# Kernel optimization log

Measured on AMD Instinct MI355X. Metric: run time of the kernel, lower is better.

## Reference

```python
import jax, jax.numpy as jnp
import numpy as np

NUM_PERIODS = 24


def setup_inputs() -> dict:
    key = jax.random.key(0)
    ks = jax.random.split(key, 12)
    B, N, F, H, E = 32, 1024, 128, 64, 16
    scale = 1.0 / np.sqrt(F)
    inp = {
        "input_features": jax.random.normal(ks[0], (B, N, F), jnp.float32),
        "cycle_indices": jax.random.randint(ks[1], (B,), 0, NUM_PERIODS, jnp.int64),
        "weight": jax.random.normal(ks[2], (F, F), jnp.float32) * scale,
        "bias": jnp.zeros((F,), jnp.float32),
        "src_emb": jax.random.normal(ks[3], (NUM_PERIODS, N, H), jnp.float32) * 0.1,
        "tgt_emb": jax.random.normal(ks[4], (NUM_PERIODS, N, H), jnp.float32) * 0.1,
        "env_W": jax.random.normal(ks[5], (E, H), jnp.float32) * (1.0 / np.sqrt(E)),
        "env_b": jnp.zeros((H,), jnp.float32),
        "res_W": jax.random.normal(ks[6], (F, F), jnp.float32) * scale,
        "res_b": jnp.zeros((F,), jnp.float32),
        "static_adj": (jax.random.uniform(ks[7], (N, N)) < 0.05).astype(jnp.float32),
        "env_features": jax.random.normal(ks[8], (N, E), jnp.float32),
    }
    return inp


def reference(input_features, cycle_indices, weight, bias, src_emb, tgt_emb,
              env_W, env_b, res_W, res_b, static_adj, env_features):
    # env encoder: Linear + ReLU (dropout is identity at inference)
    env_emb = jax.nn.relu(env_features @ env_W + env_b)            # [N, H]

    # per-period adaptive adjacency, masked by static sparsity pattern
    src = src_emb + env_emb                                        # [P, N, H]
    tgt = tgt_emb + env_emb                                        # [P, N, H]
    scores = jnp.einsum('pnh,pmh->pnm', src, tgt)                  # [P, N, N]
    adj = jax.nn.relu(scores) * static_adj                         # [P, N, N]

    period = (cycle_indices % NUM_PERIODS).astype(jnp.int32)       # [B]
    adj_b = adj[period]                                            # [B, N, N]

    support = jnp.einsum('bnd,dm->bnm', input_features, weight)    # [B, N, F]
    convolved = jnp.einsum('bnm,bmf->bnf', adj_b, support) + bias  # [B, N, F]

    residual = jax.nn.relu(input_features @ res_W + res_b)         # [B, N, F]
    return jax.nn.relu(convolved + residual)
```

## Files before the change

kernel.cpp:

```cpp
#include <hip/hip_runtime.h>
#include <hip/hip_bf16.h>

#define NPER 24
#define B_ 32
#define N_ 1024
#define F_ 128
#define H_ 64
#define E_ 16

typedef __attribute__((ext_vector_type(8))) short short8;
typedef __attribute__((ext_vector_type(4))) float f32x4;

#define GLD16(g, l) __builtin_amdgcn_global_load_lds( \
    (const __attribute__((address_space(1))) void*)(g), \
    (__attribute__((address_space(3))) void*)(l), 16, 0, 0)

static __device__ __forceinline__ unsigned short f2bf(float x) {
    union { float f; unsigned u; } v; v.f = x;
    unsigned r = v.u + 0x7fffu + ((v.u >> 16) & 1u);
    return (unsigned short)(r >> 16);
}
static __device__ __forceinline__ float bf2f(unsigned short h) {
    union { unsigned u; float f; } v; v.u = ((unsigned)h) << 16; return v.f;
}
static __device__ __forceinline__ unsigned short f2bf_hw(float x) {
    __hip_bfloat16 h = __float2bfloat16(x);
    return *(unsigned short*)&h;
}

__global__ __launch_bounds__(256) void prep_all(
    const float* __restrict__ src_emb, const float* __restrict__ tgt_emb,
    const float* __restrict__ env_features, const float* __restrict__ env_W,
    const float* __restrict__ env_b,
    const float* __restrict__ adj, const float* __restrict__ W,
    const float* __restrict__ rW, const float* __restrict__ x,
    unsigned short* __restrict__ src_bf, unsigned short* __restrict__ tgt_bf,
    unsigned short* __restrict__ adj_bf, unsigned short* __restrict__ Wt,
    unsigned short* __restrict__ rWt, unsigned short* __restrict__ x_bf)
{
    const int bid = blockIdx.x;
    if (bid < 1536) {
        const int g   = bid >> 8;
        const int idx = (bid & 255) * 256 + threadIdx.x;
        const int n = idx >> 6, h = idx & 63;
        float e = env_b[h];
#pragma unroll
        for (int k = 0; k < E_; ++k)
            e = fmaf(env_features[n * E_ + k], env_W[k * H_ + h], e);
        e = fmaxf(e, 0.f);
#pragma unroll
        for (int pp = 0; pp < 4; ++pp) {
            const size_t off = (size_t)(g * 4 + pp) * (N_ * H_) + idx;
            src_bf[off] = f2bf(src_emb[off] + e);
            tgt_bf[off] = f2bf(tgt_emb[off] + e);
        }
    } else if (bid < 2560) {
        const size_t i = ((size_t)(bid - 1536) * 256 + threadIdx.x) * 4;
        float4 v = *(const float4*)(adj + i);
        ushort4 o;
        o.x = f2bf(v.x); o.y = f2bf(v.y); o.z = f2bf(v.z); o.w = f2bf(v.w);
        *(ushort4*)(adj_bf + i) = o;
    } else if (bid < 2688) {
        const int idx = (bid - 2560) * 256 + threadIdx.x;
        const int which = idx >> 14, j = idx & 16383;
        const int f = j >> 7, d = j & 127;
        if (which == 0) Wt[f * 128 + d]  = f2bf(W[d * 128 + f]);
        else            rWt[f * 128 + d] = f2bf(rW[d * 128 + f]);
    } else {
        const size_t i = ((size_t)(bid - 2688) * 256 + threadIdx.x) * 4;
        float4 v = *(const float4*)(x + i);
        ushort4 o;
        o.x = f2bf(v.x); o.y = f2bf(v.y); o.z = f2bf(v.z); o.w = f2bf(v.w);
        *(ushort4*)(x_bf + i) = o;
    }
}

__global__ __launch_bounds__(256, 2) void gemm2_mfma(
    const unsigned short* __restrict__ x_bf,
    const unsigned short* __restrict__ Wt,
    const unsigned short* __restrict__ rWt,
    const float* __restrict__ rb,
    unsigned short* __restrict__ supT,
    unsigned short* __restrict__ resid)
{
    __shared__ unsigned short s_w[128 * 128] __attribute__((aligned(16)));
    __shared__ unsigned short s_r[128 * 128] __attribute__((aligned(16)));
    __shared__ unsigned short s_x[64 * 128]  __attribute__((aligned(16)));

    const int t = threadIdx.x, w = t >> 6, l = t & 63;
    const int ln = l & 15, kb = l >> 4;
    const size_t row0 = (size_t)blockIdx.x * 64;
    const int b   = (int)(row0 >> 10);
    const int mg0 = (int)(row0 & 1023);

#pragma unroll
    for (int j = 0; j < 8; ++j) {
        const int te = j * 256 + t;
        const int r = te >> 4, c = te & 15;
        GLD16(Wt  + (size_t)r * 128 + (c ^ (r & 7)) * 8, &s_w[te * 8]);
        GLD16(rWt + (size_t)r * 128 + (c ^ (r & 7)) * 8, &s_r[te * 8]);
    }
#pragma unroll
    for (int j = 0; j < 4; ++j) {
        const int te = j * 256 + t;
        const int r = te >> 4, c = te & 15;
        GLD16(x_bf + row0 * 128 + (size_t)r * 128 + (c ^ (r & 7)) * 8,
              &s_x[te * 8]);
    }
    asm volatile("s_waitcnt vmcnt(0) lgkmcnt(0)" ::: "memory");
    __builtin_amdgcn_s_barrier();

    f32x4 accS[8], accR[8];
#pragma unroll
    for (int q = 0; q < 8; ++q) { accS[q] = (f32x4){0,0,0,0}; accR[q] = (f32x4){0,0,0,0}; }

    const int xr = w * 16 + ln;
#pragma unroll
    for (int k = 0; k < 4; ++k) {
        short8 xa = *(const short8*)(&s_x[xr * 128 + ((k * 4 + kb) ^ (xr & 7)) * 8]);
#pragma unroll
        for (int ff = 0; ff < 8; ++ff) {
            const int fr = ff * 16 + ln;
            short8 wa = *(const short8*)(&s_w[fr * 128 + ((k * 4 + kb) ^ (fr & 7)) * 8]);
            short8 wb = *(const short8*)(&s_r[fr * 128 + ((k * 4 + kb) ^ (fr & 7)) * 8]);
            accS[ff] = __builtin_amdgcn_mfma_f32_16x16x32_bf16(wa, xa, accS[ff], 0, 0, 0);
            accR[ff] = __builtin_amdgcn_mfma_f32_16x16x32_bf16(xa, wb, accR[ff], 0, 0, 0);
        }
    }

#pragma unroll
    for (int ff = 0; ff < 8; ++ff) {
        const int m = mg0 + w * 16 + ln;
#pragma unroll
        for (int i = 0; i < 4; ++i) {
            const int f = ff * 16 + kb * 4 + i;
            supT[((size_t)b * 128 + f) * 1024 + m] = f2bf(accS[ff][i]);
        }
    }
#pragma unroll
    for (int ff = 0; ff < 8; ++ff) {
        const int f = ff * 16 + ln;
        const float rbf = rb[f];
#pragma unroll
        for (int i = 0; i < 4; ++i) {
            const size_t row = row0 + w * 16 + kb * 4 + i;
            resid[row * 128 + f] = f2bf(fmaxf(accR[ff][i] + rbf, 0.f));
        }
    }
}

__global__ __launch_bounds__(256, 2) void conv_mfma(
    const unsigned short* __restrict__ src_bf,
    const unsigned short* __restrict__ tgt_bf,
    const unsigned short* __restrict__ adj_bf,
    const unsigned short* __restrict__ supT,
    const unsigned short* __restrict__ resid,
    const float* __restrict__ bias,
    const int* __restrict__ cyc,
    float* __restrict__ out)
{
    __shared__ unsigned short s_tgt[2][64 * 64] __attribute__((aligned(16)));
    __shared__ unsigned short s_sup[2][128 * 64] __attribute__((aligned(16)));
    __shared__ unsigned short s_a[64][72] __attribute__((aligned(16)));

    const int i = blockIdx.x;
    const int work = (i & 7) * 64 + (i >> 3);
    const int b  = work >> 4;
    const int n0 = (work & 15) * 64;

    const int t = threadIdx.x, w = t >> 6, l = t & 63;
    const int ln = l & 15, kb = l >> 4;
    const int p = ((cyc[b] % NPER) + NPER) % NPER;

    const int sn = w >> 1, sm = w & 1;
    const int cf = w;

    short8 sfrag[2][2];
#pragma unroll
    for (int nt = 0; nt < 2; ++nt)
#pragma unroll
        for (int k2 = 0; k2 < 2; ++k2)
            sfrag[nt][k2] = *(const short8*)(
                src_bf + ((size_t)p * N_ + n0 + sn * 32 + nt * 16 + ln) * H_ + k2 * 32 + kb * 8);

    const unsigned short* tgtg = tgt_bf + (size_t)p * N_ * H_;
    const unsigned short* supg = supT + (size_t)b * F_ * N_;

    f32x4 acc[4][2];
#pragma unroll
    for (int q = 0; q < 4; ++q)
#pragma unroll
        for (int fb = 0; fb < 2; ++fb) acc[q][fb] = (f32x4){0, 0, 0, 0};

    auto stage = [&](int buf, int m0) {
#pragma unroll
        for (int j = 0; j < 2; ++j) {
            const int te = j * 256 + t;
            const int r = te >> 3, c = te & 7;
            GLD16(tgtg + (size_t)(m0 + r) * H_ + (c ^ (r & 7)) * 8,
                  &s_tgt[buf][te * 8]);
        }
#pragma unroll
        for (int j = 0; j < 4; ++j) {
            const int te = j * 256 + t;
            const int r = te >> 3, c = te & 7;
            GLD16(supg + (size_t)r * N_ + m0 + (c ^ (r & 7)) * 8,
                  &s_sup[buf][te * 8]);
        }
    };

    auto loadAdj = [&](int m0, ushort4 (&av)[2][2]) {
#pragma unroll
        for (int nt = 0; nt < 2; ++nt)
#pragma unroll
            for (int mt = 0; mt < 2; ++mt)
                av[nt][mt] = *(const ushort4*)(
                    adj_bf + (size_t)(n0 + sn * 32 + nt * 16 + ln) * N_
                           + m0 + sm * 32 + mt * 16 + kb * 4);
    };

    auto score = [&](int buf, const ushort4 (&av)[2][2]) {
        short8 tf[2][2];
#pragma unroll
        for (int mt = 0; mt < 2; ++mt)
#pragma unroll
            for (int k2 = 0; k2 < 2; ++k2) {
                const int trow = sm * 32 + mt * 16 + ln;
                tf[mt][k2] = *(const short8*)(
                    &s_tgt[buf][trow * 64 + ((k2 * 4 + kb) ^ (trow & 7)) * 8]);
            }
#pragma unroll
        for (int nt = 0; nt < 2; ++nt)
#pragma unroll
            for (int mt = 0; mt < 2; ++mt) {
                f32x4 c = (f32x4){0, 0, 0, 0};
                c = __builtin_amdgcn_mfma_f32_16x16x32_bf16(tf[mt][0], sfrag[nt][0], c, 0, 0, 0);
                c = __builtin_amdgcn_mfma_f32_16x16x32_bf16(tf[mt][1], sfrag[nt][1], c, 0, 0, 0);
                const int nl = sn * 32 + nt * 16 + ln;
                const int ml = sm * 32 + mt * 16 + kb * 4;
                const ushort4 a = av[nt][mt];
                uint2 q;
                q.x = (unsigned)f2bf_hw(fmaxf(c[0], 0.f) * bf2f(a.x))
                    | ((unsigned)f2bf_hw(fmaxf(c[1], 0.f) * bf2f(a.y)) << 16);
                q.y = (unsigned)f2bf_hw(fmaxf(c[2], 0.f) * bf2f(a.z))
                    | ((unsigned)f2bf_hw(fmaxf(c[3], 0.f) * bf2f(a.w)) << 16);
                *(uint2*)(&s_a[nl][ml]) = q;
            }
    };

    auto conv = [&](int buf) {
#pragma unroll
        for (int ks = 0; ks < 2; ++ks) {
            short8 bfrag[2];
#pragma unroll
            for (int fb = 0; fb < 2; ++fb) {
                const int frow = cf * 32 + fb * 16 + ln;
                bfrag[fb] = *(const short8*)(
                    &s_sup[buf][frow * 64 + ((ks * 4 + kb) ^ (frow & 7)) * 8]);
            }
#pragma unroll
            for (int nt2 = 0; nt2 < 4; ++nt2) {
                short8 af = *(const short8*)(&s_a[nt2 * 16 + ln][ks * 32 + kb * 8]);
#pragma unroll
                for (int fb = 0; fb < 2; ++fb)
                    acc[nt2][fb] = __builtin_amdgcn_mfma_f32_16x16x32_bf16(
                        af, bfrag[fb], acc[nt2][fb], 0, 0, 0);
            }
        }
    };

    auto bar_lgkm = []() {
        asm volatile("s_waitcnt lgkmcnt(0)" ::: "memory");
        __builtin_amdgcn_s_barrier();
    };
    auto bar_vm0 = []() {
        asm volatile("s_waitcnt vmcnt(0) lgkmcnt(0)" ::: "memory");
        __builtin_amdgcn_s_barrier();
    };

    ushort4 avA[2][2], avB[2][2];

    stage(0, 0);
    loadAdj(0, avA);
    bar_vm0();

    for (int tt = 0; tt < 16; tt += 2) {
        stage(1, (tt + 1) * 64);
        loadAdj((tt + 1) * 64, avB);
        score(0, avA);
        bar_lgkm();
        conv(0);
        bar_vm0();

        if (tt + 2 < 16) {
            stage(0, (tt + 2) * 64);
            loadAdj((tt + 2) * 64, avA);
        }
        score(1, avB);
        bar_lgkm();
        conv(1);
        bar_vm0();
    }

#pragma unroll
    for (int nt2 = 0; nt2 < 4; ++nt2)
#pragma unroll
    for (int fb = 0; fb < 2; ++fb) {
        const int f = cf * 32 + fb * 16 + ln;
        const float bi = bias[f];
#pragma unroll
        for (int ii = 0; ii < 4; ++ii) {
            const int n = n0 + nt2 * 16 + kb * 4 + ii;
            const size_t o = ((size_t)b * N_ + n) * F_ + f;
            out[o] = fmaxf(acc[nt2][fb][ii] + bi + bf2f(resid[o]), 0.f);
        }
    }
}

extern "C" void kernel_launch(void* const* d_in, const int* in_sizes, int n_in,
                              void* d_out, int out_size, void* d_ws, size_t ws_size,
                              hipStream_t stream) {
    const float* input_features = (const float*)d_in[0];
    const int*   cycle_indices  = (const int*)  d_in[1];
    const float* weight         = (const float*)d_in[2];
    const float* bias           = (const float*)d_in[3];
    const float* src_emb        = (const float*)d_in[4];
    const float* tgt_emb        = (const float*)d_in[5];
    const float* env_W          = (const float*)d_in[6];
    const float* env_b          = (const float*)d_in[7];
    const float* res_W          = (const float*)d_in[8];
    const float* res_b          = (const float*)d_in[9];
    const float* static_adj     = (const float*)d_in[10];
    const float* env_features   = (const float*)d_in[11];
    float* out = (float*)d_out;

    char* wsb = (char*)d_ws;
    unsigned short* src_bf = (unsigned short*)wsb;
    unsigned short* tgt_bf = src_bf + (size_t)NPER * N_ * H_;
    unsigned short* Wt     = tgt_bf + (size_t)NPER * N_ * H_;
    unsigned short* rWt    = Wt + 16384;
    unsigned short* supT   = rWt + 16384;
    unsigned short* resid  = supT + (size_t)B_ * F_ * N_;
    unsigned short* adj_bf = resid + (size_t)B_ * N_ * F_;
    unsigned short* x_bf   = adj_bf + (size_t)N_ * N_;

    prep_all<<<6784, 256, 0, stream>>>(
        src_emb, tgt_emb, env_features, env_W, env_b,
        static_adj, weight, res_W, input_features,
        src_bf, tgt_bf, adj_bf, Wt, rWt, x_bf);

    gemm2_mfma<<<(B_ * N_) / 64, 256, 0, stream>>>(
        x_bf, Wt, rWt, res_b, supT, resid);

    conv_mfma<<<512, 256, 0, stream>>>(
        src_bf, tgt_bf, adj_bf, supT, resid, bias, cycle_indices, out);
}
```

Measured before the change: 54.58 us.

## Shrink conv K-tile to 32 with 4-stage LDS ring and vmcnt-based prefetch

The fused score+conv kernel now uses 32-wide m tiles instead of 64 and keeps four LDS stages instead of two. Loads for tile c+2 are issued while tile c is computed, and a partial s_waitcnt vmcnt replaces full vmcnt(0) drains. Launch bounds move to 3 blocks per SM so that more waves fit per CU. This aims to hide global-load latency and raise occupancy, at the cost of twice as many barriers per unit of work, smaller MFMA batches per stage, and reliance on exact vmcnt accounting.

```diff
diff --git a/kernel.cpp b/kernel.cpp
--- a/kernel.cpp
+++ b/kernel.cpp
@@ -149,7 +149,7 @@
     }
 }
 
-__global__ __launch_bounds__(256, 2) void conv_mfma(
+__global__ __launch_bounds__(256, 3) void conv_mfma(
     const unsigned short* __restrict__ src_bf,
     const unsigned short* __restrict__ tgt_bf,
     const unsigned short* __restrict__ adj_bf,
@@ -159,9 +159,9 @@
     const int* __restrict__ cyc,
     float* __restrict__ out)
 {
-    __shared__ unsigned short s_tgt[2][64 * 64] __attribute__((aligned(16)));
-    __shared__ unsigned short s_sup[2][128 * 64] __attribute__((aligned(16)));
-    __shared__ unsigned short s_a[64][72] __attribute__((aligned(16)));
+    __shared__ unsigned short s_tgt[4][32 * 64]  __attribute__((aligned(16)));
+    __shared__ unsigned short s_sup[4][128 * 32] __attribute__((aligned(16)));
+    __shared__ unsigned short s_a[64][36]        __attribute__((aligned(16)));
 
     const int i = blockIdx.x;
     const int work = (i & 7) * 64 + (i >> 3);
@@ -193,113 +193,112 @@
         for (int fb = 0; fb < 2; ++fb) acc[q][fb] = (f32x4){0, 0, 0, 0};
 
     auto stage = [&](int buf, int m0) {
+        {
+            const int r = t >> 3, c = t & 7;
+            GLD16(tgtg + (size_t)(m0 + r) * H_ + (c ^ (r & 7)) * 8,
+                  &s_tgt[buf][t * 8]);
+        }
 #pragma unroll
         for (int j = 0; j < 2; ++j) {
             const int te = j * 256 + t;
-            const int r = te >> 3, c = te & 7;
-            GLD16(tgtg + (size_t)(m0 + r) * H_ + (c ^ (r & 7)) * 8,
-                  &s_tgt[buf][te * 8]);
-        }
-#pragma unroll
-        for (int j = 0; j < 4; ++j) {
-            const int te = j * 256 + t;
-            const int r = te >> 3, c = te & 7;
-            GLD16(supg + (size_t)r * N_ + m0 + (c ^ (r & 7)) * 8,
+            const int r = te >> 2, c = te & 3;
+            GLD16(supg + (size_t)r * N_ + m0 + (c ^ ((r >> 1) & 3)) * 8,
                   &s_sup[buf][te * 8]);
         }
     };
 
-    auto loadAdj = [&](int m0, ushort4 (&av)[2][2]) {
+    auto loadAdj = [&](int m0, ushort4 (&av)[2]) {
 #pragma unroll
         for (int nt = 0; nt < 2; ++nt)
-#pragma unroll
-            for (int mt = 0; mt < 2; ++mt)
-                av[nt][mt] = *(const ushort4*)(
-                    adj_bf + (size_t)(n0 + sn * 32 + nt * 16 + ln) * N_
-                           + m0 + sm * 32 + mt * 16 + kb * 4);
-    };
-
-    auto score = [&](int buf, const ushort4 (&av)[2][2]) {
-        short8 tf[2][2];
-#pragma unroll
-        for (int mt = 0; mt < 2; ++mt)
-#pragma unroll
-            for (int k2 = 0; k2 < 2; ++k2) {
-                const int trow = sm * 32 + mt * 16 + ln;
-                tf[mt][k2] = *(const short8*)(
-                    &s_tgt[buf][trow * 64 + ((k2 * 4 + kb) ^ (trow & 7)) * 8]);
-            }
-#pragma unroll
-        for (int nt = 0; nt < 2; ++nt)
-#pragma unroll
-            for (int mt = 0; mt < 2; ++mt) {
-                f32x4 c = (f32x4){0, 0, 0, 0};
-                c = __builtin_amdgcn_mfma_f32_16x16x32_bf16(tf[mt][0], sfrag[nt][0], c, 0, 0, 0);
-                c = __builtin_amdgcn_mfma_f32_16x16x32_bf16(tf[mt][1], sfrag[nt][1], c, 0, 0, 0);
-                const int nl = sn * 32 + nt * 16 + ln;
-                const int ml = sm * 32 + mt * 16 + kb * 4;
-                const ushort4 a = av[nt][mt];
-                uint2 q;
-                q.x = (unsigned)f2bf_hw(fmaxf(c[0], 0.f) * bf2f(a.x))
-                    | ((unsigned)f2bf_hw(fmaxf(c[1], 0.f) * bf2f(a.y)) << 16);
-                q.y = (unsigned)f2bf_hw(fmaxf(c[2], 0.f) * bf2f(a.z))
-                    | ((unsigned)f2bf_hw(fmaxf(c[3], 0.f) * bf2f(a.w)) << 16);
-                *(uint2*)(&s_a[nl][ml]) = q;
-            }
+            av[nt] = *(const ushort4*)(
+                adj_bf + (size_t)(n0 + sn * 32 + nt * 16 + ln) * N_
+                       + m0 + sm * 16 + kb * 4);
+    };
+
+    auto score = [&](int buf, const ushort4 (&av)[2]) {
+        const int trow = sm * 16 + ln;
+        short8 tf0 = *(const short8*)(
+            &s_tgt[buf][trow * 64 + ((kb) ^ (trow & 7)) * 8]);
+        short8 tf1 = *(const short8*)(
+            &s_tgt[buf][trow * 64 + ((4 + kb) ^ (trow & 7)) * 8]);
+#pragma unroll
+        for (int nt = 0; nt < 2; ++nt) {
+            f32x4 c = (f32x4){0, 0, 0, 0};
+            c = __builtin_amdgcn_mfma_f32_16x16x32_bf16(tf0, sfrag[nt][0], c, 0, 0, 0);
+            c = __builtin_amdgcn_mfma_f32_16x16x32_bf16(tf1, sfrag[nt][1], c, 0, 0, 0);
+            const int nl = sn * 32 + nt * 16 + ln;
+            const int ml = sm * 16 + kb * 4;
+            const ushort4 a = av[nt];
+            uint2 q;
+            q.x = (unsigned)f2bf_hw(fmaxf(c[0], 0.f) * bf2f(a.x))
+                | ((unsigned)f2bf_hw(fmaxf(c[1], 0.f) * bf2f(a.y)) << 16);
+            q.y = (unsigned)f2bf_hw(fmaxf(c[2], 0.f) * bf2f(a.z))
+                | ((unsigned)f2bf_hw(fmaxf(c[3], 0.f) * bf2f(a.w)) << 16);
+            *(uint2*)(&s_a[nl][ml]) = q;
+        }
     };
 
     auto conv = [&](int buf) {
-#pragma unroll
-        for (int ks = 0; ks < 2; ++ks) {
-            short8 bfrag[2];
-#pragma unroll
-            for (int fb = 0; fb < 2; ++fb) {
-                const int frow = cf * 32 + fb * 16 + ln;
-                bfrag[fb] = *(const short8*)(
-                    &s_sup[buf][frow * 64 + ((ks * 4 + kb) ^ (frow & 7)) * 8]);
-            }
-#pragma unroll
-            for (int nt2 = 0; nt2 < 4; ++nt2) {
-                short8 af = *(const short8*)(&s_a[nt2 * 16 + ln][ks * 32 + kb * 8]);
-#pragma unroll
-                for (int fb = 0; fb < 2; ++fb)
-                    acc[nt2][fb] = __builtin_amdgcn_mfma_f32_16x16x32_bf16(
-                        af, bfrag[fb], acc[nt2][fb], 0, 0, 0);
-            }
-        }
-    };
-
+        short8 bfrag[2];
+#pragma unroll
+        for (int fb = 0; fb < 2; ++fb) {
+            const int frow = cf * 32 + fb * 16 + ln;
+            bfrag[fb] = *(const short8*)(
+                &s_sup[buf][frow * 32 + ((kb) ^ ((frow >> 1) & 3)) * 8]);
+        }
+#pragma unroll
+        for (int nt2 = 0; nt2 < 4; ++nt2) {
+            short8 af = *(const short8*)(&s_a[nt2 * 16 + ln][kb * 8]);
+#pragma unroll
+            for (int fb = 0; fb < 2; ++fb)
+                acc[nt2][fb] = __builtin_amdgcn_mfma_f32_16x16x32_bf16(
+                    af, bfrag[fb], acc[nt2][fb], 0, 0, 0);
+        }
+    };
+
+    auto bar = []() { __builtin_amdgcn_s_barrier(); };
     auto bar_lgkm = []() {
         asm volatile("s_waitcnt lgkmcnt(0)" ::: "memory");
         __builtin_amdgcn_s_barrier();
     };
-    auto bar_vm0 = []() {
-        asm volatile("s_waitcnt vmcnt(0) lgkmcnt(0)" ::: "memory");
-        __builtin_amdgcn_s_barrier();
-    };
-
-    ushort4 avA[2][2], avB[2][2];
-
-    stage(0, 0);
-    loadAdj(0, avA);
-    bar_vm0();
-
-    for (int tt = 0; tt < 16; tt += 2) {
-        stage(1, (tt + 1) * 64);
-        loadAdj((tt + 1) * 64, avB);
-        score(0, avA);
-        bar_lgkm();
-        conv(0);
-        bar_vm0();
-
-        if (tt + 2 < 16) {
-            stage(0, (tt + 2) * 64);
-            loadAdj((tt + 2) * 64, avA);
-        }
-        score(1, avB);
-        bar_lgkm();
-        conv(1);
-        bar_vm0();
+
+    ushort4 av[4][2];
+
+    stage(0, 0);        loadAdj(0, av[0]);
+    stage(1, 32);       loadAdj(32, av[1]);
+
+#pragma unroll 1
+    for (int k = 0; k < 7; ++k) {
+        const int c0 = k * 4;
+#pragma unroll
+        for (int u = 0; u < 4; ++u) {
+            const int c = c0 + u;
+            stage((u + 2) & 3, (c + 2) * 32);
+            loadAdj((c + 2) * 32, av[(u + 2) & 3]);
+            __builtin_amdgcn_sched_barrier(0);
+            asm volatile("s_waitcnt vmcnt(10)" ::: "memory");
+            bar();
+            score(u & 3, av[u & 3]);
+            bar_lgkm();
+            conv(u & 3);
+        }
+    }
+    {
+        stage(2, 30 * 32);  loadAdj(30 * 32, av[2]);
+        __builtin_amdgcn_sched_barrier(0);
+        asm volatile("s_waitcnt vmcnt(10)" ::: "memory");
+        bar(); score(0, av[0]); bar_lgkm(); conv(0);
+
+        stage(3, 31 * 32);  loadAdj(31 * 32, av[3]);
+        __builtin_amdgcn_sched_barrier(0);
+        asm volatile("s_waitcnt vmcnt(10)" ::: "memory");
+        bar(); score(1, av[1]); bar_lgkm(); conv(1);
+
+        asm volatile("s_waitcnt vmcnt(5)" ::: "memory");
+        bar(); score(2, av[2]); bar_lgkm(); conv(2);
+
+        asm volatile("s_waitcnt vmcnt(0)" ::: "memory");
+        bar(); score(3, av[3]); bar_lgkm(); conv(3);
     }
 
 #pragma unroll
```

After: 56.17 us. 1.03x slower.
